# Kernel tuning notes

Hardware: AMD Instinct MI355X
Metric: run time of the kernel (lower is better)

## Reference

```python
import jax, jax.numpy as jnp
import numpy as np

PIXELS_PER_CELL = (8, 8)
CELLS_PER_BLOCK = (2, 2)
ORIENTATIONS = 9
GRAY_W = jnp.array([0.2125, 0.7154, 0.0721], dtype=jnp.float32)  # skimage rgb2gray
EPS = 1e-5  # skimage L2-Hys eps


def setup_inputs() -> dict:
    key = jax.random.key(0)
    x = jax.random.uniform(key, (64, 512, 512, 3), dtype=jnp.float32)
    return {"x": x}


def _hog(x):
    # rgb2gray
    gray = jnp.einsum("bhwc,c->bhw", x, GRAY_W)  # [B,H,W]
    B, H, W = gray.shape
    pr, pc = PIXELS_PER_CELL
    br, bc = CELLS_PER_BLOCK
    O = ORIENTATIONS

    # skimage _hog_channel_gradient: central differences, zero at borders
    g_row = jnp.zeros_like(gray).at[:, 1:-1, :].set(gray[:, 2:, :] - gray[:, :-2, :])
    g_col = jnp.zeros_like(gray).at[:, :, 1:-1].set(gray[:, :, 2:] - gray[:, :, :-2])

    mag = jnp.hypot(g_row, g_col)
    ori = jnp.rad2deg(jnp.arctan2(g_row, g_col)) % 180.0  # unsigned orientation

    ncr, ncc = H // pr, W // pc
    mag = mag[:, : ncr * pr, : ncc * pc]
    ori = ori[:, : ncr * pr, : ncc * pc]

    spacing = 180.0 / O
    cell_area = float(pr * pc)
    # per-orientation-bin cell histograms: hard binning (skimage cell_hog)
    hists = []
    for o in range(O):
        lo, hi = spacing * o, spacing * (o + 1)
        contrib = jnp.where((ori >= lo) & (ori < hi), mag, 0.0)
        # sum over each pr x pc cell, divide by cell area
        h = contrib.reshape(B, ncr, pr, ncc, pc).sum(axis=(2, 4)) / cell_area
        hists.append(h)
    hist = jnp.stack(hists, axis=-1)  # [B, ncr, ncc, O]

    # overlapping blocks of cells, stride 1 cell
    nbr, nbc = ncr - br + 1, ncc - bc + 1
    block = jnp.stack(
        [jnp.stack([hist[:, r : r + nbr, c : c + nbc, :] for c in range(bc)], axis=3)
         for r in range(br)], axis=3)  # [B, nbr, nbc, br, bc, O]

    # L2-Hys normalization (skimage default block_norm)
    norm = jnp.sqrt(jnp.sum(block * block, axis=(3, 4, 5), keepdims=True) + EPS ** 2)
    blk = jnp.minimum(block / norm, 0.2)
    norm2 = jnp.sqrt(jnp.sum(blk * blk, axis=(3, 4, 5), keepdims=True) + EPS ** 2)
    blk = blk / norm2

    return blk.reshape(B, -1).astype(jnp.float32)


def reference(x):
    return _hog(x)
```

## Files before the change

### kernel.cpp

```cpp
#include <hip/hip_runtime.h>
#include <math.h>

#define IMG_H 512
#define IMG_W 512
#define NCELL 64
#define NORI 9

__device__ __forceinline__ float fdlibm_atanf_inl(float x) {
#pragma clang fp contract(off)
    const float one = 1.0f;
    int hx = __float_as_int(x);
    int ix = hx & 0x7fffffff;
    int id;
    if (ix >= 0x4c800000) {
        const float v = 1.5707962513e+00f + 7.5497894159e-08f;
        return (hx > 0) ? v : -v;
    }
    if (ix < 0x3ee00000) {
        if (ix < 0x39800000) return x;
        id = -1;
    } else {
        x = fabsf(x);
        if (ix < 0x3f980000) {
            if (ix < 0x3f300000) { id = 0; x = (2.0f * x - one) / (2.0f + x); }
            else                 { id = 1; x = (x - one) / (x + one); }
        } else {
            if (ix < 0x401c0000) { id = 2; x = (x - 1.5f) / (one + 1.5f * x); }
            else                 { id = 3; x = -1.0f / x; }
        }
    }
    float z = x * x;
    float w = z * z;
    float s1 = z * (3.3333334327e-01f + w * (1.4285714924e-01f + w * (9.0908870101e-02f
             + w * (6.6610731184e-02f + w * (4.9768779427e-02f + w * 1.6285819933e-02f)))));
    float s2 = w * (-2.0000000298e-01f + w * (-1.1111110449e-01f + w * (-7.6918758452e-02f
             + w * (-5.8335702866e-02f + w * -3.6531571299e-02f))));
    if (id < 0) return x - x * (s1 + s2);
    const float hi = (id == 0) ? 4.6364760399e-01f : (id == 1) ? 7.8539812565e-01f
                   : (id == 2) ? 9.8279368877e-01f : 1.5707962513e+00f;
    const float lo = (id == 0) ? 5.0121582440e-09f : (id == 1) ? 3.7748947079e-08f
                   : (id == 2) ? 3.4473217170e-08f : 7.5497894159e-08f;
    z = hi - ((x * (s1 + s2) - lo) - x);
    return (hx < 0) ? -z : z;
}

__device__ __forceinline__ int fdlibm_bin_inl(float y, float x) {
#pragma clang fp contract(off)
    const float tiny   = 1.0e-30f;
    const float pi_o_2 = 1.5707963705e+00f;
    const float pi     = 3.1415927410e+00f;
    const float pi_lo  = -8.7422776573e-08f;

    int hx = __float_as_int(x), ix = hx & 0x7fffffff;
    int hy = __float_as_int(y), iy = hy & 0x7fffffff;
    float th;
    if (hx == 0x3f800000) { th = fdlibm_atanf_inl(y); }
    else {
        int m = ((hy >> 31) & 1) | ((hx >> 30) & 2);
        if (iy == 0) {
            switch (m) {
                case 0:
                case 1: th = y; break;
                case 2: th =  pi + tiny; break;
                default: th = -pi - tiny; break;
            }
        } else if (ix == 0) {
            th = (hy < 0) ? -pi_o_2 - tiny : pi_o_2 + tiny;
        } else {
            int k = (iy - ix) >> 23;
            float z;
            int mm = m;
            if (k > 26) {
                z = pi_o_2 + 0.5f * pi_lo;
                mm &= 1;
            } else if (k < -26 && hx < 0) {
                z = 0.0f;
            } else {
                z = fdlibm_atanf_inl(fabsf(y / x));
            }
            switch (mm) {
                case 0:  th = z; break;
                case 1:  th = -z; break;
                case 2:  th = pi - (z - pi_lo); break;
                default: th = (z - pi_lo) - pi; break;
            }
        }
    }
    const float RAD2DEG = (float)(180.0 / 3.14159265358979311600e+00);
    float m = fmodf(th * RAD2DEG, 180.0f);
    if (m < 0.0f) m += 180.0f;
    int o = (int)(m * 0.05f);
    if (o < 9) {
        if (m < 20.0f * (float)o) --o;
        else if (m >= 20.0f * (float)(o + 1)) ++o;
    }
    return o;
}

__global__ __launch_bounds__(512, 6) void hog_hist_kernel(const float* __restrict__ x,
                                                          float* __restrict__ hist) {
#pragma clang fp contract(off)
    const int bid = blockIdx.x;
    const int b   = bid >> 6;
    const int cr  = bid & 63;
    const int t   = threadIdx.x;
    const int h0  = cr * 8;

    __shared__ __align__(16) float4 raw[1920];
    __shared__ __align__(16) float  g[10][IMG_W];

    const float GW0 = 0.2125f, GW1 = 0.7154f, GW2 = 0.0721f;

#pragma unroll
    for (int p = 0; p < 2; ++p) {
        for (int i = t; i < 1920; i += 512) {
            const int rr  = i / 384;
            const int idx = i - rr * 384;
            int h = h0 - 1 + p * 5 + rr;
            if (h < 0)   h = 1;
            if (h > 511) h = 510;
            raw[i] = ((const float4*)x)[(size_t)(b * IMG_H + h) * 384 + idx];
        }
        __syncthreads();
        const float* rf = (const float*)raw;
#pragma unroll
        for (int k = 0; k < 5; ++k) {
            const float r_ = rf[k * 1536 + 3 * t + 0];
            const float g_ = rf[k * 1536 + 3 * t + 1];
            const float b_ = rf[k * 1536 + 3 * t + 2];
            g[p * 5 + k][t] = __builtin_fmaf(b_, GW2, __builtin_fmaf(g_, GW1, r_ * GW0));
        }
        __syncthreads();
    }

    const int w   = t;
    const int wl  = (w == 0)   ? 0   : w - 1;
    const int wr  = (w == 511) ? 511 : w + 1;
    const bool wok = (w >= 1) && (w <= 510);
    const int c   = w >> 3;
    const int jl  = t & 7;

    float cc[10], ee[8], ww[8];
#pragma unroll
    for (int i = 0; i < 10; ++i) cc[i] = g[i][w];
#pragma unroll
    for (int i = 0; i < 8; ++i) { ee[i] = g[i + 1][wr]; ww[i] = g[i + 1][wl]; }

    const float CK[8] = { 0.9396926208f,  0.7660444431f,  0.5f,            0.1736481777f,
                         -0.1736481777f, -0.5f,           -0.7660444431f, -0.9396926208f };
    const float SK[8] = { 0.3420201433f,  0.6427876097f,  0.8660254038f,  0.9848077530f,
                          0.9848077530f,  0.8660254038f,  0.6427876097f,  0.3420201433f };

    float bh[9];
#pragma unroll
    for (int k = 0; k < 9; ++k) bh[k] = 0.0f;

    int   nsus = 0;
    float s0gr = 0.0f, s0gc = 0.0f, s0mag = 0.0f;
    float s1gr = 0.0f, s1gc = 0.0f, s1mag = 0.0f;

#pragma unroll
    for (int r = 0; r < 8; ++r) {
        const float gr = cc[r + 2] - cc[r];
        const float gc = wok ? (ee[r] - ww[r]) : 0.0f;
        const float mag = __builtin_amdgcn_sqrtf(__builtin_fmaf(gr, gr, gc * gc));

        const float gy = fabsf(gr);
        const float gx = (gr < 0.0f) ? -gc : gc;
        const float th = 1e-4f * mag;
        int  o = 0;
        bool suspect = false;
#pragma unroll
        for (int k = 0; k < 8; ++k) {
            const float ck = __builtin_fmaf(gy, CK[k], -(gx * SK[k]));
            o += (ck >= 0.0f) ? 1 : 0;
            suspect = suspect || (fabsf(ck) < th);
        }
        suspect = suspect || ((gx < 0.0f) && (gy < 1e-5f * fabsf(gc)));
        if (gy == 0.0f) { o = 0; suspect = false; }
        if (__builtin_expect(suspect, 0)) {
            if (nsus == 0)      { s0gr = gr; s0gc = gc; s0mag = mag; }
            else if (nsus == 1) { s1gr = gr; s1gc = gc; s1mag = mag; }
            ++nsus;
            o = 9;
        }
#pragma unroll
        for (int k = 0; k < 9; ++k) bh[k] += (o == k) ? mag : 0.0f;
    }

    if (__builtin_expect(nsus > 0, 0)) {
        if (nsus <= 2) {
            {
                const int o = fdlibm_bin_inl(s0gr, s0gc);
                if (o < 9) bh[o] += s0mag;
            }
            if (nsus == 2) {
                const int o = fdlibm_bin_inl(s1gr, s1gc);
                if (o < 9) bh[o] += s1mag;
            }
        } else {
            for (int r = 0; r < 8; ++r) {
                const float gr = g[r + 2][w] - g[r][w];
                const float gc = wok ? (g[r + 1][wr] - g[r + 1][wl]) : 0.0f;
                const float mag = __builtin_amdgcn_sqrtf(__builtin_fmaf(gr, gr, gc * gc));
                const float gy = fabsf(gr);
                const float gx = (gr < 0.0f) ? -gc : gc;
                const float th = 1e-4f * mag;
                bool suspect = false;
                for (int k = 0; k < 8; ++k) {
                    const float ck = __builtin_fmaf(gy, CK[k], -(gx * SK[k]));
                    suspect = suspect || (fabsf(ck) < th);
                }
                suspect = suspect || ((gx < 0.0f) && (gy < 1e-5f * fabsf(gc)));
                if (gy == 0.0f) suspect = false;
                if (suspect) {
                    const int o = fdlibm_bin_inl(gr, gc);
                    if (o < 9) bh[o] += mag;
                }
            }
        }
    }

#pragma unroll
    for (int k = 0; k < 9; ++k) {
        bh[k] += __shfl_xor(bh[k], 1, 64);
        bh[k] += __shfl_xor(bh[k], 2, 64);
        bh[k] += __shfl_xor(bh[k], 4, 64);
    }
    float mv = bh[0];
#pragma unroll
    for (int k = 1; k < 8; ++k) mv = (jl == k) ? bh[k] : mv;
    float* hout = hist + (size_t)(b * NCELL + cr) * (NCELL * NORI);
    hout[c * NORI + jl] = mv * 0.015625f;
    if (jl == 0) hout[c * NORI + 8] = bh[8] * 0.015625f;
}

__global__ __launch_bounds__(256) void hog_norm_kernel(const float* __restrict__ hist,
                                                       float* __restrict__ out) {
#pragma clang fp contract(off)
    const int bid = blockIdx.x;
    const int b   = bid / 63;
    const int r   = bid % 63;
    const int t   = threadIdx.x;
    const int c   = t >> 2;
    const int l   = t & 3;
    if (c >= 63) return;

    const int bi = l >> 1, bj = l & 1;
    const float* v = hist + ((size_t)(b * NCELL + r + bi) * NCELL + (c + bj)) * NORI;

    float vv[9];
    float ss = 0.0f;
#pragma unroll
    for (int k = 0; k < 9; ++k) { vv[k] = v[k]; ss += vv[k] * vv[k]; }
    ss += __shfl_xor(ss, 1, 64);
    ss += __shfl_xor(ss, 2, 64);
    const float rn1 = 1.0f / sqrtf(ss + 1e-10f);
    float ss2 = 0.0f;
#pragma unroll
    for (int k = 0; k < 9; ++k) { vv[k] = fminf(vv[k] * rn1, 0.2f); ss2 += vv[k] * vv[k]; }
    ss2 += __shfl_xor(ss2, 1, 64);
    ss2 += __shfl_xor(ss2, 2, 64);
    const float rn2 = 1.0f / sqrtf(ss2 + 1e-10f);

    float* od = out + (size_t)bid * (63 * 36) + (c * 36 + l * 9);
#pragma unroll
    for (int k = 0; k < 9; ++k) od[k] = vv[k] * rn2;
}

extern "C" void kernel_launch(void* const* d_in, const int* in_sizes, int n_in,
                              void* d_out, int out_size, void* d_ws, size_t ws_size,
                              hipStream_t stream) {
    const float* x = (const float*)d_in[0];
    float* out     = (float*)d_out;
    float* hist    = (float*)d_ws;

    hog_hist_kernel<<<dim3(64 * 64), dim3(512), 0, stream>>>(x, hist);
    hog_norm_kernel<<<dim3(64 * 63), dim3(256), 0, stream>>>(hist, out);
}
```

Before: 310.2 us.

## Split grayscale conversion into a separate kernel to avoid redundant RGB reads

Adds a standalone gray_kernel that converts the RGB input to grayscale once and writes it to workspace. The histogram kernel then reads 10 gray rows per cell row instead of 10 RGB rows with halo, which avoids re-reading overlapping halo rows of three-channel data and drops the two-phase staging with extra barriers. The cost is an extra launch plus a full write and read of a 64 MB grayscale intermediate through global memory.

```diff
diff --git a/kernel.cpp b/kernel.cpp
--- a/kernel.cpp
+++ b/kernel.cpp
@@ -5,6 +5,7 @@
 #define IMG_W 512
 #define NCELL 64
 #define NORI 9
+#define GRAY_OFF (4 * 1024 * 1024)
 
 __device__ __forceinline__ float fdlibm_atanf_inl(float x) {
 #pragma clang fp contract(off)
@@ -97,7 +98,28 @@
     return o;
 }
 
-__global__ __launch_bounds__(512, 6) void hog_hist_kernel(const float* __restrict__ x,
+__global__ __launch_bounds__(256) void gray_kernel(const float* __restrict__ x,
+                                                   float* __restrict__ gray) {
+#pragma clang fp contract(off)
+    __shared__ __align__(16) float4 raw[768];
+    const int bb = blockIdx.x;
+    const int t  = threadIdx.x;
+    const float4* X4 = (const float4*)x + (size_t)bb * 768;
+#pragma unroll
+    for (int k = 0; k < 3; ++k) raw[t + 256 * k] = X4[t + 256 * k];
+    __syncthreads();
+    const float* w = (const float*)raw;
+    const float GW0 = 0.2125f, GW1 = 0.7154f, GW2 = 0.0721f;
+    const int base = 12 * t;
+    float4 g4;
+    g4.x = __builtin_fmaf(w[base +  2], GW2, __builtin_fmaf(w[base +  1], GW1, w[base +  0] * GW0));
+    g4.y = __builtin_fmaf(w[base +  5], GW2, __builtin_fmaf(w[base +  4], GW1, w[base +  3] * GW0));
+    g4.z = __builtin_fmaf(w[base +  8], GW2, __builtin_fmaf(w[base +  7], GW1, w[base +  6] * GW0));
+    g4.w = __builtin_fmaf(w[base + 11], GW2, __builtin_fmaf(w[base + 10], GW1, w[base +  9] * GW0));
+    ((float4*)gray)[(size_t)bb * 256 + t] = g4;
+}
+
+__global__ __launch_bounds__(512, 6) void hog_hist_kernel(const float* __restrict__ gray,
                                                           float* __restrict__ hist) {
 #pragma clang fp contract(off)
     const int bid = blockIdx.x;
@@ -106,32 +128,16 @@
     const int t   = threadIdx.x;
     const int h0  = cr * 8;
 
-    __shared__ __align__(16) float4 raw[1920];
-    __shared__ __align__(16) float  g[10][IMG_W];
-
-    const float GW0 = 0.2125f, GW1 = 0.7154f, GW2 = 0.0721f;
-
-#pragma unroll
-    for (int p = 0; p < 2; ++p) {
-        for (int i = t; i < 1920; i += 512) {
-            const int rr  = i / 384;
-            const int idx = i - rr * 384;
-            int h = h0 - 1 + p * 5 + rr;
-            if (h < 0)   h = 1;
-            if (h > 511) h = 510;
-            raw[i] = ((const float4*)x)[(size_t)(b * IMG_H + h) * 384 + idx];
-        }
-        __syncthreads();
-        const float* rf = (const float*)raw;
-#pragma unroll
-        for (int k = 0; k < 5; ++k) {
-            const float r_ = rf[k * 1536 + 3 * t + 0];
-            const float g_ = rf[k * 1536 + 3 * t + 1];
-            const float b_ = rf[k * 1536 + 3 * t + 2];
-            g[p * 5 + k][t] = __builtin_fmaf(b_, GW2, __builtin_fmaf(g_, GW1, r_ * GW0));
-        }
-        __syncthreads();
-    }
+    __shared__ __align__(16) float g[10][IMG_W];
+
+#pragma unroll
+    for (int rr = 0; rr < 10; ++rr) {
+        int h = h0 - 1 + rr;
+        if (h < 0)   h = 1;
+        if (h > 511) h = 510;
+        g[rr][t] = gray[(size_t)(b * IMG_H + h) * IMG_W + t];
+    }
+    __syncthreads();
 
     const int w   = t;
     const int wl  = (w == 0)   ? 0   : w - 1;
@@ -274,7 +280,9 @@
     const float* x = (const float*)d_in[0];
     float* out     = (float*)d_out;
     float* hist    = (float*)d_ws;
-
-    hog_hist_kernel<<<dim3(64 * 64), dim3(512), 0, stream>>>(x, hist);
+    float* gray    = (float*)d_ws + GRAY_OFF;
+
+    gray_kernel   <<<dim3(16384),   dim3(256), 0, stream>>>(x, gray);
+    hog_hist_kernel<<<dim3(64 * 64), dim3(512), 0, stream>>>(gray, hist);
     hog_norm_kernel<<<dim3(64 * 63), dim3(256), 0, stream>>>(hist, out);
 }
```

New measurement: 343.7 us. 10.8% more time.
